# Optimization experiments

Hardware: AMD Instinct MI355X
Metric: run time of the kernel (lower is better)

## Reference

```python
import jax, jax.numpy as jnp
import numpy as np

S, FEAT, D, H, L, DFF, C = 1024, 64, 512, 8, 2, 2048, 10
DB = D // 4  # distance-bias MLP hidden
NFREQ = D // 6  # 85 -> 6*85=510 dims, padded to 512
EPS = 1e-5


def _layernorm(x, g, b):
    mu = jnp.mean(x, axis=-1, keepdims=True)
    var = jnp.mean(jnp.square(x - mu), axis=-1, keepdims=True)
    return (x - mu) * jax.lax.rsqrt(var + EPS) * g + b


def setup_inputs() -> dict:
    key = jax.random.key(0)
    ks = iter(jax.random.split(key, 40))
    def w(shape, scale=0.02):
        return (jax.random.normal(next(ks), shape, jnp.float32) * scale)
    inp = {
        'features': jax.random.normal(next(ks), (S, FEAT), jnp.float32),
        'positions': jax.random.uniform(next(ks), (S, 3), jnp.float32),
        'freq_bands': jnp.asarray(10.0 ** np.linspace(0.0, 10.0, NFREQ), jnp.float32),
        'in_w': w((FEAT, D)), 'in_b': jnp.zeros((D,), jnp.float32),
        'qw': w((L, D, D)), 'qb': jnp.zeros((L, D), jnp.float32),
        'kw': w((L, D, D)), 'kb': jnp.zeros((L, D), jnp.float32),
        'vw': w((L, D, D)), 'vb': jnp.zeros((L, D), jnp.float32),
        'ow': w((L, D, D)), 'ob': jnp.zeros((L, D), jnp.float32),
        'db1w': w((L, 1, DB), 0.5), 'db1b': jnp.zeros((L, DB), jnp.float32),
        'db2w': w((L, DB, H), 0.1), 'db2b': jnp.zeros((L, H), jnp.float32),
        'n1g': jnp.ones((L, D), jnp.float32), 'n1b': jnp.zeros((L, D), jnp.float32),
        'n2g': jnp.ones((L, D), jnp.float32), 'n2b': jnp.zeros((L, D), jnp.float32),
        'f1w': w((L, D, DFF)), 'f1b': jnp.zeros((L, DFF), jnp.float32),
        'f2w': w((L, DFF, D)), 'f2b': jnp.zeros((L, D), jnp.float32),
        'c1w': w((D, D // 2)), 'c1b': jnp.zeros((D // 2,), jnp.float32),
        'c2w': w((D // 2, C)), 'c2b': jnp.zeros((C,), jnp.float32),
    }
    return inp


def _forward(features, positions, freq_bands, in_w, in_b, qw, qb, kw, kb, vw, vb,
             ow, ob, db1w, db1b, db2w, db2b, n1g, n1b, n2g, n2b,
             f1w, f1b, f2w, f2b, c1w, c1b, c2w, c2b):
    d_model = in_w.shape[1]
    nhead = db2w.shape[-1]
    head_dim = d_model // nhead
    scale = 1.0 / np.sqrt(head_dim)

    x = features[None] @ in_w + in_b            # [1, S, D]
    pos = positions[None]                        # [1, S, 3]

    # 3D sinusoidal positional encoding: [sin0,cos0,sin1,cos1,sin2,cos2]
    enc = []
    for i in range(3):
        cs = pos[..., i:i + 1] * freq_bands      # [1, S, NFREQ] (broadcast)
        enc.append(jnp.sin(cs))
        enc.append(jnp.cos(cs))
    pe = jnp.concatenate(enc, axis=-1)           # [1, S, 6*NFREQ]
    if pe.shape[-1] > d_model:
        pe = pe[..., :d_model]
    elif pe.shape[-1] < d_model:
        pe = jnp.pad(pe, ((0, 0), (0, 0), (0, d_model - pe.shape[-1])))
    x = x + pe

    # pairwise distances [1, S, S, 1]; safe sqrt (zero grad on diagonal)
    diff = pos[:, :, None, :] - pos[:, None, :, :]
    sq = jnp.sum(jnp.square(diff), axis=-1, keepdims=True)
    dist = jnp.sqrt(jnp.where(sq > 0, sq, 1.0)) * (sq > 0)

    n_layers = qw.shape[0]
    seq = x.shape[1]
    for l in range(n_layers):
        q = (x @ qw[l] + qb[l]).reshape(1, seq, nhead, head_dim)
        k = (x @ kw[l] + kb[l]).reshape(1, seq, nhead, head_dim)
        v = (x @ vw[l] + vb[l]).reshape(1, seq, nhead, head_dim)
        scores = jnp.einsum('bihd,bjhd->bhij', q, k) * scale  # [1,H,S,S]
        hbias = jax.nn.relu(dist @ db1w[l] + db1b[l])          # [1,S,S,DB]
        bias = jnp.einsum('bijc,ch->bhij', hbias, db2w[l]) + db2b[l][None, :, None, None]
        attn = jax.nn.softmax(scores + bias, axis=-1)
        out = jnp.einsum('bhij,bjhd->bihd', attn, v).reshape(1, seq, d_model)
        out = out @ ow[l] + ob[l]
        x = _layernorm(x + out, n1g[l], n1b[l])
        ffn = jax.nn.relu(x @ f1w[l] + f1b[l]) @ f2w[l] + f2b[l]
        x = _layernorm(x + ffn, n2g[l], n2b[l])

    pooled = jnp.mean(x, axis=1)                 # [1, D]
    return jax.nn.relu(pooled @ c1w + c1b) @ c2w + c2b  # [1, C]


def reference(features, positions, freq_bands, in_w, in_b, qw, qb, kw, kb, vw, vb,
              ow, ob, db1w, db1b, db2w, db2b, n1g, n1b, n2g, n2b,
              f1w, f1b, f2w, f2b, c1w, c1b, c2w, c2b):
    return _forward(features, positions, freq_bands, in_w, in_b, qw, qb, kw, kb, vw, vb,
                    ow, ob, db1w, db1b, db2w, db2b, n1g, n1b, n2g, n2b,
                    f1w, f1b, f2w, f2b, c1w, c1b, c2w, c2b)
```

## Files before the change

### kernel.cpp

```cpp
#include <hip/hip_runtime.h>

namespace {
constexpr int kS   = 1024;
constexpr int kD   = 512;
constexpr int kDFF = 2048;
constexpr int kNF  = 85;
}

typedef __attribute__((ext_vector_type(8))) short bhalf8_t;
typedef _Float16 half8_t __attribute__((ext_vector_type(8)));
typedef __attribute__((ext_vector_type(4))) float f32x4_t;

__device__ __forceinline__ float wave_sum(float v) {
#pragma unroll
    for (int o = 1; o < 64; o <<= 1) v += __shfl_xor(v, o, 64);
    return v;
}
__device__ __forceinline__ unsigned short f2h(float f) {
    _Float16 h = (_Float16)f;
    return __builtin_bit_cast(unsigned short, h);
}
__device__ __forceinline__ float h2f(unsigned short u) {
    return (float)__builtin_bit_cast(_Float16, u);
}

__device__ __forceinline__ void tr_tile32(const float* __restrict__ in,
                                          unsigned short* __restrict__ out,
                                          int N, int K, int k0, int n0, int t,
                                          float* tile )
{
    int r = t >> 3, c4 = (t & 7) * 4;
    float4 v = *reinterpret_cast<const float4*>(&in[(long)(k0 + r) * N + n0 + c4]);
    tile[r * 33 + c4] = v.x; tile[r * 33 + c4 + 1] = v.y;
    tile[r * 33 + c4 + 2] = v.z; tile[r * 33 + c4 + 3] = v.w;
    __syncthreads();
    int nr = t >> 3, kq = (t & 7) * 4;
    unsigned short h[4];
#pragma unroll
    for (int j = 0; j < 4; ++j) h[j] = f2h(tile[(kq + j) * 33 + nr]);
    *reinterpret_cast<ushort4*>(&out[(long)(n0 + nr) * K + k0 + kq]) =
        make_ushort4(h[0], h[1], h[2], h[3]);
}

__global__ __launch_bounds__(256)
void prep_k(const float* __restrict__ feat, const float* __restrict__ pos,
            const float* __restrict__ fb, const float* __restrict__ in_w,
            const float* __restrict__ in_b, float* __restrict__ x,
            unsigned short* __restrict__ xb, float* __restrict__ dist,
            const float* __restrict__ qw, const float* __restrict__ kw,
            const float* __restrict__ vw, const float* __restrict__ ow,
            unsigned short* __restrict__ qwb, unsigned short* __restrict__ kwb,
            unsigned short* __restrict__ vwb, unsigned short* __restrict__ owb,
            const float* __restrict__ f1w, unsigned short* __restrict__ f1wb,
            const float* __restrict__ f2w, unsigned short* __restrict__ f2wb,
            const float* __restrict__ a_, const float* __restrict__ b_,
            const float* __restrict__ w2, const float* __restrict__ b2,
            float* __restrict__ bp_out, float* __restrict__ Atab,
            float* __restrict__ Btab)
{
    __shared__ float smem[1056];
    int bid = blockIdx.x;
    int t = threadIdx.x;
    if (bid < 256) {
        int s0 = bid * 4;
        smem[t] = feat[s0 * 64 + t];
        __syncthreads();
        float b0 = in_b[t], b1 = in_b[t + 256];
        float a0[4] = {b0, b0, b0, b0}, a1[4] = {b1, b1, b1, b1};
#pragma unroll 4
        for (int c = 0; c < 64; ++c) {
            float w0 = in_w[c * kD + t], w1 = in_w[c * kD + 256 + t];
#pragma unroll
            for (int r = 0; r < 4; ++r) {
                a0[r] = fmaf(smem[r * 64 + c], w0, a0[r]);
                a1[r] = fmaf(smem[r * 64 + c], w1, a1[r]);
            }
        }
#pragma unroll
        for (int r = 0; r < 4; ++r) {
            int s = s0 + r;
            float pe0 = 0.f, pe1 = 0.f;
            int d = t;
            if (d < 6 * kNF) {
                int seg = d / kNF, idx = d - seg * kNF;
                float cs = pos[s * 3 + (seg >> 1)] * fb[idx];
                pe0 = (seg & 1) ? cosf(cs) : sinf(cs);
            }
            d = t + 256;
            if (d < 6 * kNF) {
                int seg = d / kNF, idx = d - seg * kNF;
                float cs = pos[s * 3 + (seg >> 1)] * fb[idx];
                pe1 = (seg & 1) ? cosf(cs) : sinf(cs);
            }
            float o0 = a0[r] + pe0, o1 = a1[r] + pe1;
            x[s * kD + t]        = o0;
            x[s * kD + 256 + t]  = o1;
            xb[s * kD + t]       = f2h(o0);
            xb[s * kD + 256 + t] = f2h(o1);
        }
    } else if (bid < 1280) {
        int i = bid - 256;
        float px = pos[i * 3], py = pos[i * 3 + 1], pz = pos[i * 3 + 2];
        for (int j = t; j < kS; j += 256) {
            float dx = px - pos[j * 3], dy = py - pos[j * 3 + 1], dz = pz - pos[j * 3 + 2];
            float sq = dx * dx + dy * dy + dz * dz;
            dist[(long)i * kS + j] = sq > 0.f ? sqrtf(sq) : 0.f;
        }
    } else if (bid < 7424) {
        int idx = bid - 1280;
        if (idx < 2048) {
            int zz = idx >> 8, rem = idx & 255;
            int mat = zz >> 1, layer = zz & 1;
            const float* in = (mat == 0) ? qw : (mat == 1) ? kw : (mat == 2) ? vw : ow;
            unsigned short* out = (mat == 0) ? qwb : (mat == 1) ? kwb : (mat == 2) ? vwb : owb;
            tr_tile32(in + (long)layer * 262144, out + (long)layer * 262144,
                      512, 512, (rem & 15) * 32, (rem >> 4) * 32, t, smem);
        } else if (idx < 4096) {
            int l = idx - 2048;
            int z = l >> 10;
            tr_tile32(f1w + (long)z * 1048576, f1wb + (long)z * 1048576,
                      2048, 512, (l & 15) * 32, ((l >> 4) & 63) * 32, t, smem);
        } else {
            int l = idx - 4096;
            int z = l >> 10;
            tr_tile32(f2w + (long)z * 1048576, f2wb + (long)z * 1048576,
                      512, 2048, (l & 63) * 32, ((l >> 6) & 15) * 32, t, smem);
        }
    } else {
        int l = bid - 7424;
        int seg = l % 129, ly = l / 129;
        const float* ap = a_ + ly * 128;
        const float* bpp = b_ + ly * 128;
        const float* w2p = w2 + ly * 1024;
        const float* b2p = b2 + ly * 8;
        float* At = Atab + ly * 1040;
        float* Bt = Btab + ly * 1040;

        if (t < 128) {
            float a = ap[t], b = bpp[t];
            smem[t] = (a != 0.f) ? (-b / a) : 3.0e38f;
        }
        __syncthreads();
        for (int ksz = 2; ksz <= 128; ksz <<= 1) {
            for (int j = ksz >> 1; j > 0; j >>= 1) {
                if (t < 128) {
                    int ixj = t ^ j;
                    if (ixj > t) {
                        bool up = ((t & ksz) == 0);
                        float x0 = smem[t], x1 = smem[ixj];
                        if ((x0 > x1) == up) { smem[t] = x1; smem[ixj] = x0; }
                    }
                }
                __syncthreads();
            }
        }
        float m;
        if (seg == 0)        m = smem[0] - 1.0f;
        else if (seg == 128) m = smem[127] + 1.0f;
        else                 m = 0.5f * (smem[seg - 1] + smem[seg]);
        if (seg == 0 && t < 128) bp_out[ly * 128 + t] = smem[t];
        __syncthreads();

        int h = t & 7, cg = t >> 3;
        float A = 0.f, B = 0.f;
#pragma unroll
        for (int j = 0; j < 4; ++j) {
            int c = cg * 4 + j;
            float a = ap[c], b = bpp[c];
            if (fmaf(a, m, b) > 0.f) {
                float w = w2p[c * 8 + h];
                A = fmaf(a, w, A);
                B = fmaf(b, w, B);
            }
        }
#pragma unroll
        for (int off = 8; off < 64; off <<= 1) {
            A += __shfl_xor(A, off, 64);
            B += __shfl_xor(B, off, 64);
        }
        int w = t >> 6, lane = t & 63;
        if (lane < 8) { smem[w * 8 + lane] = A; smem[32 + w * 8 + lane] = B; }
        __syncthreads();
        if (t < 8) {
            float At_ = smem[t] + smem[8 + t] + smem[16 + t] + smem[24 + t];
            float Bt_ = smem[32 + t] + smem[40 + t] + smem[48 + t] + smem[56 + t];
            At[seg * 8 + t] = At_;
            Bt[seg * 8 + t] = Bt_ + b2p[t];
        }
    }
}

constexpr int BKp = 72;
constexpr int ASZ = 64 * BKp;
constexpr int BSZ = 128 * BKp;

template<int K>
__device__ __forceinline__ void gemm_core(
    const unsigned short* __restrict__ Ap, const unsigned short* __restrict__ Bp,
    int lda, int ldb, int bm, int bn, int tid,
    unsigned short* __restrict__ As, unsigned short* __restrict__ Bs,
    f32x4_t acc[2][4])
{
    int w = tid >> 6, lane = tid & 63, quad = lane >> 4, l16 = lane & 15;
    int wm = (w >> 1) * 32, wn = (w & 1) * 64;
    int ar = tid >> 2, ac = (tid & 3) * 16;
    int br = tid >> 1, bc = (tid & 1) * 32;
    const unsigned short* pa = Ap + (long)(bm + ar) * lda + ac;
    const unsigned short* pb = Bp + (long)(bn + br) * ldb + bc;

    bhalf8_t a0_0, a0_1, b0_0, b0_1, b0_2, b0_3;
    bhalf8_t a1_0, a1_1, b1_0, b1_1, b1_2, b1_3;

#define LDG(S, k0) do { \
    a##S##_0 = *reinterpret_cast<const bhalf8_t*>(pa + (k0)); \
    a##S##_1 = *reinterpret_cast<const bhalf8_t*>(pa + (k0) + 8); \
    b##S##_0 = *reinterpret_cast<const bhalf8_t*>(pb + (k0)); \
    b##S##_1 = *reinterpret_cast<const bhalf8_t*>(pb + (k0) + 8); \
    b##S##_2 = *reinterpret_cast<const bhalf8_t*>(pb + (k0) + 16); \
    b##S##_3 = *reinterpret_cast<const bhalf8_t*>(pb + (k0) + 24); } while (0)
#define STG(S, as, bs) do { \
    *reinterpret_cast<bhalf8_t*>(&(as)[ar * BKp + ac])      = a##S##_0; \
    *reinterpret_cast<bhalf8_t*>(&(as)[ar * BKp + ac + 8])  = a##S##_1; \
    *reinterpret_cast<bhalf8_t*>(&(bs)[br * BKp + bc])      = b##S##_0; \
    *reinterpret_cast<bhalf8_t*>(&(bs)[br * BKp + bc + 8])  = b##S##_1; \
    *reinterpret_cast<bhalf8_t*>(&(bs)[br * BKp + bc + 16]) = b##S##_2; \
    *reinterpret_cast<bhalf8_t*>(&(bs)[br * BKp + bc + 24]) = b##S##_3; } while (0)

    constexpr int NT = K / 64;
    LDG(0, 0);
    STG(0, As, Bs);
    if (NT > 1) LDG(1, 64);
#pragma unroll
    for (int t = 0; t < NT; ++t) {
        __syncthreads();
        if (t + 2 < NT) {
            if ((t & 1) == 0) LDG(0, (t + 2) * 64);
            else              LDG(1, (t + 2) * 64);
        }
        const unsigned short* as = As + (t & 1) * ASZ;
        const unsigned short* bs = Bs + (t & 1) * BSZ;
#pragma unroll
        for (int kq = 0; kq < 2; ++kq) {
            bhalf8_t af[2], bf[4];
#pragma unroll
            for (int i = 0; i < 2; ++i)
                af[i] = *reinterpret_cast<const bhalf8_t*>(
                    &as[(wm + i * 16 + l16) * BKp + kq * 32 + quad * 8]);
#pragma unroll
            for (int j = 0; j < 4; ++j)
                bf[j] = *reinterpret_cast<const bhalf8_t*>(
                    &bs[(wn + j * 16 + l16) * BKp + kq * 32 + quad * 8]);
#pragma unroll
            for (int i = 0; i < 2; ++i)
#pragma unroll
                for (int j = 0; j < 4; ++j)
                    acc[i][j] = __builtin_amdgcn_mfma_f32_16x16x32_f16(
                        __builtin_bit_cast(half8_t, af[i]), __builtin_bit_cast(half8_t, bf[j]),
                        acc[i][j], 0, 0, 0);
        }
        if (t + 1 < NT) {
            if (((t + 1) & 1) == 0) STG(0, As, Bs);
            else                    STG(1, As + ASZ, Bs + BSZ);
        }
    }
#undef LDG
#undef STG
}

__global__ __launch_bounds__(256, 2)
void qkv_bias_k(const unsigned short* __restrict__ xb,
                const unsigned short* __restrict__ qwb, const unsigned short* __restrict__ kwb,
                const unsigned short* __restrict__ vwb,
                const float* __restrict__ qbias, const float* __restrict__ kbias,
                const float* __restrict__ vbias,
                unsigned short* __restrict__ qb2, unsigned short* __restrict__ kb2,
                unsigned short* __restrict__ vtb,
                const float* __restrict__ dist, const float* __restrict__ bp,
                const float* __restrict__ Atab, const float* __restrict__ Btab,
                unsigned short* __restrict__ bmap, unsigned int* __restrict__ cnt)
{
    __shared__ __align__(16) unsigned short smem[2 * ASZ + 2 * BSZ];
    int bid = blockIdx.x;
    int tid = threadIdx.x;
    if (bid < 192) {
        int z = bid >> 6, rem = bid & 63;
        int bm = (rem & 15) * 64, bn = (rem >> 4) * 128;
        const unsigned short* Bp = (z == 1) ? kwb : (z == 2) ? vwb : qwb;
        const float* bias = (z == 1) ? kbias : (z == 2) ? vbias : qbias;
        f32x4_t acc[2][4] = {};
        gemm_core<512>(xb, Bp, 512, 512, bm, bn, tid, smem, smem + 2 * ASZ, acc);

        int w = tid >> 6, lane = tid & 63, quad = lane >> 4, l16 = lane & 15;
        int wm = (w >> 1) * 32, wn = (w & 1) * 64;
        if (z == 2) {
            __syncthreads();
            unsigned short* T = smem;
#pragma unroll
            for (int j = 0; j < 4; ++j) {
                int ln = wn + j * 16 + l16;
                float bv = bias[bn + ln];
#pragma unroll
                for (int i = 0; i < 2; ++i)
#pragma unroll
                    for (int r = 0; r < 4; ++r)
                        T[ln * BKp + wm + i * 16 + quad * 4 + r] =
                            f2h((acc[i][j][r] + bv) * 1024.f);
            }
            __syncthreads();
            int nr = tid >> 1, mc = (tid & 1) * 32;
            int gn = bn + nr;
            unsigned short* dst = vtb + (long)(gn >> 6) * 65536
                                + (long)(gn & 63) * 1024 + bm + mc;
#pragma unroll
            for (int jj = 0; jj < 4; ++jj)
                *reinterpret_cast<bhalf8_t*>(dst + jj * 8) =
                    *reinterpret_cast<const bhalf8_t*>(&T[nr * BKp + mc + jj * 8]);
        } else {
#pragma unroll
            for (int j = 0; j < 4; ++j) {
                int n = bn + wn + j * 16 + l16;
                float bv = bias[n];
                unsigned short* dst = ((z == 1) ? kb2 : qb2)
                    + (long)(n >> 6) * 131072 + (n & 63);
#pragma unroll
                for (int i = 0; i < 2; ++i)
#pragma unroll
                    for (int r = 0; r < 4; ++r) {
                        int m = bm + wm + i * 16 + quad * 4 + r;
                        float s = acc[i][j][r] + bv;
                        unsigned short hi = f2h(s);
                        dst[(long)m * 128]      = hi;
                        dst[(long)m * 128 + 64] = (z == 0) ? f2h(s - h2f(hi)) : hi;
                    }
            }
        }
    } else {
        if (bid == 192 && tid < 8) cnt[tid] = 0;
        float* fs = reinterpret_cast<float*>(smem);
        float* bps = fs;
        float* Ah  = fs + 128;
        float* Bh  = fs + 1160;
        int t = tid;
        if (t < 128) bps[t] = bp[t];
        for (int i = t; i < 1032; i += 256) { Ah[i] = Atab[i]; Bh[i] = Btab[i]; }
        __syncthreads();
        long i = ((long)(bid - 192) * 256 + t) * 4;
        float4 d4 = *reinterpret_cast<const float4*>(dist + i);
        float dv[4] = {d4.x, d4.y, d4.z, d4.w};
        int seg[4];
#pragma unroll
        for (int j = 0; j < 4; ++j) {
            float tv = dv[j];
            int lo = 0, hi = 128;
            while (lo < hi) { int mid = (lo + hi) >> 1; if (bps[mid] < tv) lo = mid + 1; else hi = mid; }
            seg[j] = lo;
        }
        long gm  = i >> 10;
        int gn0  = (int)(i & 1023);
        int zz   = gn0 >> 7, nb = (gn0 >> 4) & 7, c4 = gn0 & 15;
        long pbase = gm * 1024 + zz * 128 + nb;
#pragma unroll
        for (int h = 0; h < 8; ++h) {
            unsigned short* bh = bmap + (long)h * 1048576 + pbase;
#pragma unroll
            for (int j = 0; j < 4; ++j)
                bh[(c4 + j) * 8] =
                    f2h(fmaf(Ah[seg[j] * 8 + h], dv[j], Bh[seg[j] * 8 + h]));
        }
    }
}

__global__ __launch_bounds__(256, 2)
void bgemm_ffn1_k(const unsigned short* __restrict__ A,
                  const unsigned short* __restrict__ B,
                  const float* __restrict__ bias,
                  unsigned short* __restrict__ hb)
{
    __shared__ __align__(16) unsigned short smem[2 * ASZ + 2 * BSZ];
    int tid = threadIdx.x;
    int bm = blockIdx.x * 64, bn = blockIdx.y * 128;
    f32x4_t acc[2][4] = {};
    gemm_core<512>(A, B, 512, 512, bm, bn, tid, smem, smem + 2 * ASZ, acc);

    int w = tid >> 6, lane = tid & 63, quad = lane >> 4, l16 = lane & 15;
    int wm = (w >> 1) * 32, wn = (w & 1) * 64;
#pragma unroll
    for (int j = 0; j < 4; ++j) {
        int n = bn + wn + j * 16 + l16;
        float bv = bias[n];
#pragma unroll
        for (int i = 0; i < 2; ++i)
#pragma unroll
            for (int r = 0; r < 4; ++r) {
                int m = bm + wm + i * 16 + quad * 4 + r;
                hb[(long)m * kDFF + n] = f2h(fmaxf(acc[i][j][r] + bv, 0.f));
            }
    }
}

template<int K>
__global__ __launch_bounds__(256, 2)
void bgemm_k(const unsigned short* __restrict__ A, const unsigned short* __restrict__ B,
             int N, int lda, int ldb, unsigned short* __restrict__ Cpart)
{
    __shared__ __align__(16) unsigned short smem[2 * ASZ + 2 * BSZ];
    int tid = threadIdx.x;
    int ks = blockIdx.z;
    const unsigned short* Ap = A + (long)ks * K;
    const unsigned short* Bp = B + (long)ks * K;
    int bm = blockIdx.x * 64, bn = blockIdx.y * 128;
    f32x4_t acc[2][4] = {};
    gemm_core<K>(Ap, Bp, lda, ldb, bm, bn, tid, smem, smem + 2 * ASZ, acc);

    int w = tid >> 6, lane = tid & 63, quad = lane >> 4, l16 = lane & 15;
    int wm = (w >> 1) * 32, wn = (w & 1) * 64;
    unsigned short* Cp = Cpart + (long)ks * kS * N;
#pragma unroll
    for (int i = 0; i < 2; ++i)
#pragma unroll
        for (int j = 0; j < 4; ++j)
#pragma unroll
            for (int r = 0; r < 4; ++r) {
                int m = bm + wm + i * 16 + quad * 4 + r;
                int n = bn + wn + j * 16 + l16;
                Cp[(long)m * N + n] = f2h(acc[i][j][r]);
            }
}

__global__ __launch_bounds__(256, 2)
void bgemm_oproj_k(const unsigned short* __restrict__ po,
                   const float* __restrict__ pm, const float* __restrict__ pl,
                   const unsigned short* __restrict__ Bw,
                   unsigned short* __restrict__ Cpart)
{
    __shared__ __align__(16) unsigned short As[2 * ASZ];
    __shared__ __align__(16) unsigned short Bs[2 * BSZ];
    __shared__ float wz_s[2][64][9];
    __shared__ float inv_s[2][64];

    int tid = threadIdx.x;
    int ks = blockIdx.z;
    int bm = blockIdx.x * 64, bn = blockIdx.y * 128;
    int h0 = ks * 2;

    int br = tid >> 1, bc = (tid & 1) * 32;
    {
        const unsigned short* pb = Bw + (long)(bn + br) * 512 + ks * 128 + bc;
#pragma unroll
        for (int t = 0; t < 2; ++t) {
            bhalf8_t v0 = *reinterpret_cast<const bhalf8_t*>(pb + t * 64);
            bhalf8_t v1 = *reinterpret_cast<const bhalf8_t*>(pb + t * 64 + 8);
            bhalf8_t v2 = *reinterpret_cast<const bhalf8_t*>(pb + t * 64 + 16);
            bhalf8_t v3 = *reinterpret_cast<const bhalf8_t*>(pb + t * 64 + 24);
            unsigned short* bs = Bs + t * BSZ;
            *reinterpret_cast<bhalf8_t*>(&bs[br * BKp + bc])      = v0;
            *reinterpret_cast<bhalf8_t*>(&bs[br * BKp + bc + 8])  = v1;
            *reinterpret_cast<bhalf8_t*>(&bs[br * BKp + bc + 16]) = v2;
            *reinterpret_cast<bhalf8_t*>(&bs[br * BKp + bc + 24]) = v3;
        }
    }

    if (tid < 128) {
        int t = tid >> 6, r = tid & 63;
        long sidx = (long)(h0 + t) * 1024 + bm + r;
        float m[8], M = -3.0e38f;
#pragma unroll
        for (int z = 0; z < 8; ++z) { m[z] = pm[z * 8192 + sidx]; M = fmaxf(M, m[z]); }
        float lt = 0.f;
#pragma unroll
        for (int z = 0; z < 8; ++z) {
            float w = __expf(m[z] - M);
            wz_s[t][r][z] = w;
            lt = fmaf(pl[z * 8192 + sidx], w, lt);
        }
        inv_s[t][r] = 1.f / lt;
    }
    __syncthreads();

    int ar = tid >> 2, ac = (tid & 3) * 16;
#pragma unroll
    for (int t = 0; t < 2; ++t) {
        float inv = inv_s[t][ar];
        const unsigned short* p = po + ((long)(h0 + t) * 1024 + bm + ar) * 64 + ac;
        float acc[16] = {};
#pragma unroll
        for (int z = 0; z < 8; ++z) {
            float w = wz_s[t][ar][z];
            bhalf8_t v0 = *reinterpret_cast<const bhalf8_t*>(p + (long)z * 524288);
            bhalf8_t v1 = *reinterpret_cast<const bhalf8_t*>(p + (long)z * 524288 + 8);
#pragma unroll
            for (int j = 0; j < 8; ++j) {
                acc[j]     = fmaf(h2f((unsigned short)v0[j]), w, acc[j]);
                acc[8 + j] = fmaf(h2f((unsigned short)v1[j]), w, acc[8 + j]);
            }
        }
        unsigned short* as = As + t * ASZ;
#pragma unroll
        for (int j = 0; j < 16; ++j)
            as[ar * BKp + ac + j] = f2h(acc[j] * inv);
    }
    __syncthreads();

    int w = tid >> 6, lane = tid & 63, quad = lane >> 4, l16 = lane & 15;
    int wm = (w >> 1) * 32, wn = (w & 1) * 64;
    f32x4_t accf[2][4] = {};
#pragma unroll
    for (int t = 0; t < 2; ++t) {
        const unsigned short* as = As + t * ASZ;
        const unsigned short* bs = Bs + t * BSZ;
#pragma unroll
        for (int kq = 0; kq < 2; ++kq) {
            bhalf8_t af[2], bf[4];
#pragma unroll
            for (int i = 0; i < 2; ++i)
                af[i] = *reinterpret_cast<const bhalf8_t*>(
                    &as[(wm + i * 16 + l16) * BKp + kq * 32 + quad * 8]);
#pragma unroll
            for (int j = 0; j < 4; ++j)
                bf[j] = *reinterpret_cast<const bhalf8_t*>(
                    &bs[(wn + j * 16 + l16) * BKp + kq * 32 + quad * 8]);
#pragma unroll
            for (int i = 0; i < 2; ++i)
#pragma unroll
                for (int j = 0; j < 4; ++j)
                    accf[i][j] = __builtin_amdgcn_mfma_f32_16x16x32_f16(
                        __builtin_bit_cast(half8_t, af[i]), __builtin_bit_cast(half8_t, bf[j]),
                        accf[i][j], 0, 0, 0);
        }
    }

    unsigned short* Cp = Cpart + (long)ks * kS * 512;
#pragma unroll
    for (int i = 0; i < 2; ++i)
#pragma unroll
        for (int j = 0; j < 4; ++j)
#pragma unroll
            for (int r = 0; r < 4; ++r) {
                int m = bm + wm + i * 16 + quad * 4 + r;
                int n = bn + wn + j * 16 + l16;
                Cp[(long)m * 512 + n] = f2h(accf[i][j][r]);
            }
}

__global__ __launch_bounds__(256, 3)
void flash_part_k(const unsigned short* __restrict__ qb2, const unsigned short* __restrict__ kb2,
                  const unsigned short* __restrict__ vtb, const unsigned short* __restrict__ bmap,
                  unsigned short* __restrict__ po, float* __restrict__ pm, float* __restrict__ pl)
{
    constexpr int KP = 136;
    __shared__ __align__(16) unsigned short Klds[128 * KP];
    __shared__ __align__(16) unsigned short Vlds[64 * KP];

    int tid = threadIdx.x;
    int w    = tid >> 6;
    int lane = tid & 63;
    int quad = lane >> 4, l16 = lane & 15;

    int wg  = blockIdx.x;
    int lin = (wg & 7) * 128 + (wg >> 3);
    int qbg = lin & 15;
    int h   = (lin >> 4) & 7;
    int z   = lin >> 7;
    int qb  = qbg * 4 + w;
    int bm  = qb * 16;
    int k0  = z * 128;

    const unsigned short* Qh = qb2 + (long)h * 131072;
    const unsigned short* Kh = kb2 + (long)h * 131072;
    const unsigned short* Vh = vtb + (long)h * 65536;
    const unsigned short* Bm = bmap + (long)h * 1048576;

    {
        int kr = tid >> 1, kc = (tid & 1) * 64;
#pragma unroll
        for (int j = 0; j < 8; ++j)
            *reinterpret_cast<bhalf8_t*>(&Klds[kr * KP + kc + j * 8]) =
                *reinterpret_cast<const bhalf8_t*>(&Kh[(long)(k0 + kr) * 128 + kc + j * 8]);
        int vr = tid >> 2, vc = (tid & 3) * 32;
#pragma unroll
        for (int j = 0; j < 4; ++j)
            *reinterpret_cast<bhalf8_t*>(&Vlds[vr * KP + vc + j * 8]) =
                *reinterpret_cast<const bhalf8_t*>(&Vh[(long)vr * 1024 + k0 + vc + j * 8]);
    }

    bhalf8_t aq[4];
#pragma unroll
    for (int kq = 0; kq < 4; ++kq)
        aq[kq] = *reinterpret_cast<const bhalf8_t*>(
            &Qh[(long)(bm + l16) * 128 + kq * 32 + quad * 8]);
    bhalf8_t bias8[4];
#pragma unroll
    for (int r = 0; r < 4; ++r) {
        int gm = bm + quad * 4 + r;
        bias8[r] = *reinterpret_cast<const bhalf8_t*>(
            &Bm[(long)gm * 1024 + z * 128 + l16 * 8]);
    }

    __syncthreads();

    f32x4_t sacc[8] = {};
#pragma unroll
    for (int kq = 0; kq < 4; ++kq) {
        bhalf8_t bk[8];
#pragma unroll
        for (int nb = 0; nb < 8; ++nb)
            bk[nb] = *reinterpret_cast<const bhalf8_t*>(
                &Klds[(nb * 16 + l16) * KP + kq * 32 + quad * 8]);
#pragma unroll
        for (int nb = 0; nb < 8; ++nb)
            sacc[nb] = __builtin_amdgcn_mfma_f32_16x16x32_f16(
                __builtin_bit_cast(half8_t, aq[kq]), __builtin_bit_cast(half8_t, bk[nb]),
                sacc[nb], 0, 0, 0);
    }

    float m_r[4] = {-3.0e38f, -3.0e38f, -3.0e38f, -3.0e38f};
#pragma unroll
    for (int nb = 0; nb < 8; ++nb)
#pragma unroll
        for (int r = 0; r < 4; ++r) {
            float bias = h2f((unsigned short)bias8[r][nb]);
            float s = fmaf(sacc[nb][r], 0.125f, bias);
            sacc[nb][r] = s;
            m_r[r] = fmaxf(m_r[r], s);
        }
#pragma unroll
    for (int r = 0; r < 4; ++r) {
        float m_ = m_r[r];
#pragma unroll
        for (int off = 1; off < 16; off <<= 1) m_ = fmaxf(m_, __shfl_xor(m_, off, 64));
        m_r[r] = m_;
    }

    __syncthreads();

    unsigned short* Ps = Klds + w * 16 * KP;
    float l_r[4];
#pragma unroll
    for (int r = 0; r < 4; ++r) {
        int row = quad * 4 + r;
        float mN = m_r[r];
        float s_ = 0.f;
#pragma unroll
        for (int nb = 0; nb < 8; ++nb) {
            float p = __expf(sacc[nb][r] - mN);
            Ps[row * KP + nb * 16 + l16] = f2h(p * 16384.f);
            s_ += p;
        }
#pragma unroll
        for (int off = 1; off < 16; off <<= 1) s_ += __shfl_xor(s_, off, 64);
        l_r[r] = s_;
    }

    long sbase = (((long)z * 8 + h) * 64 + qb) * 16;
    if (l16 == 0) {
#pragma unroll
        for (int r = 0; r < 4; ++r) {
            pm[sbase + quad * 4 + r] = m_r[r];
            pl[sbase + quad * 4 + r] = l_r[r];
        }
    }

    f32x4_t oacc[4] = {};
#pragma unroll
    for (int kq2 = 0; kq2 < 4; ++kq2) {
        bhalf8_t ap = *reinterpret_cast<const bhalf8_t*>(&Ps[l16 * KP + kq2 * 32 + quad * 8]);
#pragma unroll
        for (int j2 = 0; j2 < 4; ++j2) {
            bhalf8_t bv = *reinterpret_cast<const bhalf8_t*>(
                &Vlds[(j2 * 16 + l16) * KP + kq2 * 32 + quad * 8]);
            oacc[j2] = __builtin_amdgcn_mfma_f32_16x16x32_f16(
                __builtin_bit_cast(half8_t, ap), __builtin_bit_cast(half8_t, bv),
                oacc[j2], 0, 0, 0);
        }
    }

    unsigned short* pob = po + sbase * 64;
#pragma unroll
    for (int j2 = 0; j2 < 4; ++j2)
#pragma unroll
        for (int r = 0; r < 4; ++r)
            pob[(quad * 4 + r) * 64 + j2 * 16 + l16] =
                f2h(oacc[j2][r] * (1.f / 16777216.f));
}

__global__ __launch_bounds__(256)
void add_ln_fused_k(const unsigned short* __restrict__ part, float* __restrict__ x,
                    const float* __restrict__ bias,
                    const float* __restrict__ g, const float* __restrict__ b,
                    unsigned short* __restrict__ xb, int splitk)
{
    __shared__ float sm[4];
    int row = blockIdx.x, t = threadIdx.x;
    const long MN = (long)kS * kD;
    float* xr = x + (long)row * kD;
    float s0 = 0.f, s1 = 0.f;
    const unsigned short* pr = part + (long)row * kD;
    for (int sl = 0; sl < splitk; ++sl) {
        s0 += h2f(pr[(long)sl * MN + t]);
        s1 += h2f(pr[(long)sl * MN + t + 256]);
    }
    s0 += bias[t] + xr[t];
    s1 += bias[t + 256] + xr[t + 256];
    float sum = wave_sum(s0 + s1);
    if ((t & 63) == 0) sm[t >> 6] = sum;
    __syncthreads();
    sum = sm[0] + sm[1] + sm[2] + sm[3];
    float mu = sum * (1.f / kD);
    float d0 = s0 - mu, d1 = s1 - mu;
    __syncthreads();
    float vs = wave_sum(d0 * d0 + d1 * d1);
    if ((t & 63) == 0) sm[t >> 6] = vs;
    __syncthreads();
    vs = sm[0] + sm[1] + sm[2] + sm[3];
    float rs = rsqrtf(vs * (1.f / kD) + 1e-5f);
    float o0 = fmaf(d0 * rs, g[t], b[t]);
    float o1 = fmaf(d1 * rs, g[t + 256], b[t + 256]);
    xr[t]       = o0;
    xr[t + 256] = o1;
    unsigned short* xrow = xb + (long)row * 512;
    xrow[t]       = f2h(o0);
    xrow[t + 256] = f2h(o1);
}

__global__ __launch_bounds__(256)
void pool_head_k(const float* __restrict__ x, float* __restrict__ partial,
                 unsigned int* __restrict__ cnt2,
                 const float* __restrict__ c1w, const float* __restrict__ c1b,
                 const float* __restrict__ c2w, const float* __restrict__ c2b,
                 float* __restrict__ out)
{
    __shared__ float pooled[kD];
    __shared__ float h1[256];
    __shared__ int isLast;
    int t = threadIdx.x;
    int cb = blockIdx.x & 1, rb = blockIdx.x >> 1;
    int col = cb * 256 + t;
    float s = 0.f;
    for (int r = rb * 128; r < rb * 128 + 128; ++r) s += x[(long)r * kD + col];
    partial[rb * kD + col] = s;

    __threadfence();
    if (t == 0) isLast = (atomicAdd(cnt2, 1u) == 15u);
    __syncthreads();
    if (!isLast) return;
    __threadfence();

    for (int d = t; d < kD; d += 256) {
        float ps = 0.f;
        for (int r = 0; r < 8; ++r) ps += partial[r * kD + d];
        pooled[d] = ps * (1.0f / kS);
    }
    __syncthreads();
    float acc = c1b[t];
    for (int f = 0; f < kD; ++f) acc = fmaf(pooled[f], c1w[f * 256 + t], acc);
    h1[t] = fmaxf(acc, 0.f);
    __syncthreads();
    if (t < 10) {
        float o = c2b[t];
        for (int f = 0; f < 256; ++f) o = fmaf(h1[f], c2w[f * 10 + t], o);
        out[t] = o;
    }
}

extern "C" void kernel_launch(void* const* d_in, const int* in_sizes, int n_in,
                              void* d_out, int out_size, void* d_ws, size_t ws_size,
                              hipStream_t stream)
{
    (void)in_sizes; (void)n_in; (void)out_size; (void)ws_size;
    const float* features = (const float*)d_in[0];
    const float* positions= (const float*)d_in[1];
    const float* fb       = (const float*)d_in[2];
    const float* in_w     = (const float*)d_in[3];
    const float* in_b     = (const float*)d_in[4];
    const float* qw  = (const float*)d_in[5];
    const float* qb  = (const float*)d_in[6];
    const float* kw  = (const float*)d_in[7];
    const float* kb  = (const float*)d_in[8];
    const float* vw  = (const float*)d_in[9];
    const float* vb  = (const float*)d_in[10];
    const float* ow  = (const float*)d_in[11];
    const float* ob  = (const float*)d_in[12];
    const float* db1w= (const float*)d_in[13];
    const float* db1b= (const float*)d_in[14];
    const float* db2w= (const float*)d_in[15];
    const float* db2b= (const float*)d_in[16];
    const float* n1g = (const float*)d_in[17];
    const float* n1b = (const float*)d_in[18];
    const float* n2g = (const float*)d_in[19];
    const float* n2b = (const float*)d_in[20];
    const float* f1w = (const float*)d_in[21];
    const float* f1b = (const float*)d_in[22];
    const float* f2w = (const float*)d_in[23];
    const float* f2b = (const float*)d_in[24];
    const float* c1w = (const float*)d_in[25];
    const float* c1b = (const float*)d_in[26];
    const float* c2w = (const float*)d_in[27];
    const float* c2b = (const float*)d_in[28];

    float* ws = (float*)d_ws;
    const long SD = (long)kS * kD;
    float* x      = ws;
    float* dist   = ws + 3 * SD;
    float* part_f = ws + 5 * SD;
    float* bpw    = ws + 17 * SD;
    float* Atab   = bpw + 256;
    float* Btab   = Atab + 2080;
    float* partial= Btab + 2080;

    unsigned short* part16 = (unsigned short*)part_f;
    unsigned short* po     = (unsigned short*)part_f;
    float* pmv = part_f + 2162688;
    float* plv = pmv + 65536;
    unsigned int* cnt2 = (unsigned int*)(plv + 65536);
    unsigned short* part16b = (unsigned short*)(part_f + 2293792);

    unsigned short* ub = (unsigned short*)(ws + 17 * SD + 8512);
    unsigned short* xb   = ub;
    unsigned short* qb2  = ub   + 1048576;
    unsigned short* kb2  = qb2  + 1048576;
    unsigned short* vtb  = kb2  + 1048576;
    unsigned short* hb   = vtb  + 524288;
    unsigned short* qwb  = hb   + 2097152;
    unsigned short* kwb  = qwb  + 524288;
    unsigned short* vwb  = kwb  + 524288;
    unsigned short* owb  = vwb  + 524288;
    unsigned short* f1wb = owb  + 524288;
    unsigned short* f2wb = f1wb + 2097152;
    unsigned short* bmap = f2wb + 2097152;

    prep_k<<<7682, 256, 0, stream>>>(features, positions, fb, in_w, in_b, x, xb,
                                     dist, qw, kw, vw, ow, qwb, kwb, vwb, owb,
                                     f1w, f1wb, f2w, f2wb,
                                     db1w, db1b, db2w, db2b, bpw, Atab, Btab);

    for (int l = 0; l < 2; ++l) {
        qkv_bias_k<<<1216, 256, 0, stream>>>(
            xb, qwb + l * 262144, kwb + l * 262144, vwb + l * 262144,
            qb + l * kD, kb + l * kD, vb + l * kD, qb2, kb2, vtb,
            dist, bpw + l * 128, Atab + l * 1040, Btab + l * 1040, bmap, cnt2);

        flash_part_k<<<1024, 256, 0, stream>>>(
            qb2, kb2, vtb, bmap, po, pmv, plv);

        bgemm_oproj_k<<<dim3(16, 4, 4), 256, 0, stream>>>(
            po, pmv, plv, owb + l * 262144, part16b);
        add_ln_fused_k<<<kS, 256, 0, stream>>>(
            part16b, x, ob + l * kD, n1g + l * kD, n1b + l * kD, xb, 4);

        bgemm_ffn1_k<<<dim3(16, 16), 256, 0, stream>>>(
            xb, f1wb + l * 1048576, f1b + l * kDFF, hb);

        bgemm_k<512><<<dim3(16, 4, 4), 256, 0, stream>>>(
            hb, f2wb + l * 1048576, 512, 2048, 2048, part16);
        add_ln_fused_k<<<kS, 256, 0, stream>>>(
            part16, x, f2b + l * kD, n2g + l * kD, n2b + l * kD, xb, 4);
    }

    pool_head_k<<<16, 256, 0, stream>>>(x, partial, cnt2, c1w, c1b, c2w, c2b,
                                        (float*)d_out);
}
```

Baseline: 279.8 us.

## Spread pooled classifier first layer across all blocks with grid spin barrier

The pooling/classifier kernel used to run the whole 512x256 first classifier layer in the single last-arriving block. Now every one of the 16 blocks waits at an atomic spin barrier, recomputes the pooled vector, and computes 16 of the 256 hidden outputs using 16-lane shuffle reductions. A second counter elects the last block to do the small final layer. This removes a serial tail, but relies on all 16 blocks being co-resident for the spin barrier, and on the counters being cleared between calls.

```diff
diff --git a/kernel.cpp b/kernel.cpp
--- a/kernel.cpp
+++ b/kernel.cpp
@@ -724,41 +724,66 @@
 
 __global__ __launch_bounds__(256)
 void pool_head_k(const float* __restrict__ x, float* __restrict__ partial,
-                 unsigned int* __restrict__ cnt2,
+                 float* __restrict__ h1g, unsigned int* __restrict__ cnt2,
                  const float* __restrict__ c1w, const float* __restrict__ c1b,
                  const float* __restrict__ c2w, const float* __restrict__ c2b,
                  float* __restrict__ out)
 {
     __shared__ float pooled[kD];
-    __shared__ float h1[256];
-    __shared__ int isLast;
+    __shared__ int flag;
     int t = threadIdx.x;
-    int cb = blockIdx.x & 1, rb = blockIdx.x >> 1;
+    int bid = blockIdx.x;
+    int cb = bid & 1, rb = bid >> 1;
     int col = cb * 256 + t;
     float s = 0.f;
     for (int r = rb * 128; r < rb * 128 + 128; ++r) s += x[(long)r * kD + col];
     partial[rb * kD + col] = s;
 
     __threadfence();
-    if (t == 0) isLast = (atomicAdd(cnt2, 1u) == 15u);
-    __syncthreads();
-    if (!isLast) return;
+    if (t == 0) {
+        atomicAdd(&cnt2[0], 1u);
+        while (atomicAdd(&cnt2[0], 0u) < 16u) {}
+    }
+    __syncthreads();
     __threadfence();
 
-    for (int d = t; d < kD; d += 256) {
-        float ps = 0.f;
-        for (int r = 0; r < 8; ++r) ps += partial[r * kD + d];
-        pooled[d] = ps * (1.0f / kS);
-    }
-    __syncthreads();
-    float acc = c1b[t];
-    for (int f = 0; f < kD; ++f) acc = fmaf(pooled[f], c1w[f * 256 + t], acc);
-    h1[t] = fmaxf(acc, 0.f);
-    __syncthreads();
-    if (t < 10) {
-        float o = c2b[t];
-        for (int f = 0; f < 256; ++f) o = fmaf(h1[f], c2w[f * 10 + t], o);
-        out[t] = o;
+    {
+        float p0 = 0.f, p1 = 0.f;
+#pragma unroll
+        for (int r = 0; r < 8; ++r) {
+            p0 += partial[r * kD + t];
+            p1 += partial[r * kD + t + 256];
+        }
+        pooled[t]       = p0 * (1.0f / kS);
+        pooled[t + 256] = p1 * (1.0f / kS);
+    }
+    __syncthreads();
+
+    {
+        int c = bid * 16 + (t >> 4);
+        int sub = t & 15;
+        float a = 0.f;
+        for (int f = sub; f < kD; f += 16)
+            a = fmaf(pooled[f], c1w[(long)f * 256 + c], a);
+#pragma unroll
+        for (int o = 1; o < 16; o <<= 1) a += __shfl_xor(a, o, 64);
+        if (sub == 0) h1g[c] = fmaxf(a + c1b[c], 0.f);
+    }
+
+    __threadfence();
+    if (t == 0) flag = (atomicAdd(&cnt2[1], 1u) == 15u);
+    __syncthreads();
+    if (!flag) return;
+    __threadfence();
+
+    if (t < 160) {
+        int c = t >> 4, sub = t & 15;
+        float a = 0.f;
+        for (int f = sub; f < 256; f += 16)
+            a = fmaf(h1g[f], c2w[(long)f * 10 + c], a);
+#pragma unroll
+        for (int o = 1; o < 16; o <<= 1) a += __shfl_xor(a, o, 64);
+        if (sub == 0) out[c] = a + c2b[c];
     }
 }
 
@@ -812,7 +837,8 @@
     float* pmv = part_f + 2162688;
     float* plv = pmv + 65536;
     unsigned int* cnt2 = (unsigned int*)(plv + 65536);
-    unsigned short* part16b = (unsigned short*)(part_f + 2293792);
+    float* h1g = (float*)(cnt2 + 16);
+    unsigned short* part16b = (unsigned short*)(part_f + 2294048);
 
     unsigned short* ub = (unsigned short*)(ws + 17 * SD + 8512);
     unsigned short* xb   = ub;
@@ -856,6 +882,6 @@
             part16, x, f2b + l * kD, n2g + l * kD, n2b + l * kD, xb, 4);
     }
 
-    pool_head_k<<<16, 256, 0, stream>>>(x, partial, cnt2, c1w, c1b, c2w, c2b,
-                                        (float*)d_out);
-}
+    pool_head_k<<<16, 256, 0, stream>>>(x, partial, h1g, cnt2,
+                                        c1w, c1b, c2w, c2b, (float*)d_out);
+}
```

Result: no change. 283.5 us (+1.3%).
